# Kernel optimization log

Hardware: AMD Instinct MI355X
Metric: run time of the kernel (lower is better)

Reference implementation:

```python
import jax, jax.numpy as jnp
import numpy as np


def setup_inputs() -> dict:
    key = jax.random.key(0)
    k1, k2, k3 = jax.random.split(key, 3)
    B, C, H, W = 4, 3, 1024, 1920
    im0 = jax.random.normal(k1, (B, C, H, W), dtype=jnp.float32)
    # realistic optical-flow displacements of a few pixels
    flow = jax.random.normal(k2, (B, H, W, 2), dtype=jnp.float32) * 5.0
    flowback = jax.random.normal(k3, (B, H, W, 2), dtype=jnp.float32) * 5.0
    return {"im0": im0, "flow": flow, "flowback": flowback, "interpolation_mode": 0}


def _splat(im0, flow, interpolation_mode):
    # im0: [B,C,H,W], flow: [B,H,W,2] (dx, dy)
    B, C, H, W = im0.shape
    src = jnp.transpose(im0, (0, 2, 3, 1)).reshape(B * H * W, C)  # [BHW, C]
    gy, gx = jnp.meshgrid(jnp.arange(H, dtype=jnp.float32),
                          jnp.arange(W, dtype=jnp.float32), indexing="ij")
    x = gx[None] + flow[..., 0]  # [B,H,W] target x coord
    y = gy[None] + flow[..., 1]  # [B,H,W] target y coord
    b_idx = jnp.arange(B, dtype=jnp.int32)[:, None, None] * (H * W)  # batch offset

    out_flat = jnp.zeros((B * H * W, C), dtype=im0.dtype)

    if interpolation_mode == 1:  # Nearest
        xi = jnp.round(x).astype(jnp.int32)
        yi = jnp.round(y).astype(jnp.int32)
        corners = [(xi, yi, jnp.ones_like(x))]
    else:  # Bilinear: scatter-add to 4 neighbors
        x0 = jnp.floor(x).astype(jnp.int32)
        y0 = jnp.floor(y).astype(jnp.int32)
        x1, y1 = x0 + 1, y0 + 1
        x0f, y0f = x0.astype(x.dtype), y0.astype(y.dtype)
        wx1, wy1 = x - x0f, y - y0f
        wx0, wy0 = 1.0 - wx1, 1.0 - wy1
        corners = [(x0, y0, wx0 * wy0), (x1, y0, wx1 * wy0),
                   (x0, y1, wx0 * wy1), (x1, y1, wx1 * wy1)]

    for xi, yi, wgt in corners:
        valid = (xi >= 0) & (xi < W) & (yi >= 0) & (yi < H)
        w = wgt * valid.astype(im0.dtype)
        xc = jnp.clip(xi, 0, W - 1)
        yc = jnp.clip(yi, 0, H - 1)
        idx = (b_idx + yc * W + xc).reshape(-1)  # [BHW]
        out_flat = out_flat.at[idx].add(src * w.reshape(-1, 1))

    return jnp.transpose(out_flat.reshape(B, H, W, C), (0, 3, 1, 2))


def reference(im0, flow, flowback, interpolation_mode):
    # flowback is accepted (as in the CUDA extension signature) but the
    # forward splat itself only consumes im0 and the forward flow.
    return _splat(im0, flow, interpolation_mode)
```

## Files before the change

### kernel.cpp

```cpp
#include <hip/hip_runtime.h>

constexpr int B_ = 4;
constexpr int C_ = 3;
constexpr int H_ = 1024;
constexpr int W_ = 1920;
constexpr int HW_ = H_ * W_;

constexpr int TW = 128;
constexpr int TH = 64;
constexpr int R  = 16;
constexpr int EW = TW + 2 * R;
constexpr int EH = TH + 2 * R;
constexpr int ECELLS = EW * EH;

static_assert(W_ % TW == 0 && H_ % TH == 0, "exact tiling assumed");

__global__ __launch_bounds__(256) void forward_warp_tiled(
    const float* __restrict__ im0,
    const float2* __restrict__ flow,
    const int* __restrict__ mode_p,
    float* __restrict__ out) {
    __shared__ float tile[ECELLS];

    const int tx0 = blockIdx.x * TW;
    const int ty0 = blockIdx.y * TH;
    const int b   = blockIdx.z;
    const int mode = *mode_p;
    const int ex0 = tx0 - R;
    const int ey0 = ty0 - R;

    for (int c = 0; c < C_; ++c) {
        for (int i = threadIdx.x; i < ECELLS; i += 256) tile[i] = 0.0f;
        __syncthreads();

        const float* im0c = im0 + ((size_t)(b * C_ + c)) * HW_;
        float* outc = out + ((size_t)(b * C_ + c)) * HW_;

        for (int p = threadIdx.x; p < TW * TH; p += 256) {
            const int lx = p & (TW - 1);
            const int ly = p >> 7;
            const int x = tx0 + lx;
            const int y = ty0 + ly;
            const float2 f = flow[(size_t)(b * H_ + y) * W_ + x];
            const float s = im0c[y * W_ + x];
            const float px = (float)x + f.x;
            const float py = (float)y + f.y;

            int   cx[4], cy[4];
            float cw[4];
            int ncorn;
            if (mode == 1) {
                cx[0] = (int)rintf(px);
                cy[0] = (int)rintf(py);
                cw[0] = 1.0f;
                ncorn = 1;
            } else {
                const float xf = floorf(px), yf = floorf(py);
                const int x0 = (int)xf, y0i = (int)yf;
                const float wx1 = px - xf, wy1 = py - yf;
                const float wx0 = 1.0f - wx1, wy0 = 1.0f - wy1;
                cx[0] = x0;     cy[0] = y0i;     cw[0] = wx0 * wy0;
                cx[1] = x0 + 1; cy[1] = y0i;     cw[1] = wx1 * wy0;
                cx[2] = x0;     cy[2] = y0i + 1; cw[2] = wx0 * wy1;
                cx[3] = x0 + 1; cy[3] = y0i + 1; cw[3] = wx1 * wy1;
                ncorn = 4;
            }
            for (int k = 0; k < ncorn; ++k) {
                const int exi = cx[k] - ex0;
                const int eyi = cy[k] - ey0;
                const float v = s * cw[k];
                if ((unsigned)exi < (unsigned)EW && (unsigned)eyi < (unsigned)EH) {
                    atomicAdd(&tile[eyi * EW + exi], v);
                } else if ((unsigned)cx[k] < (unsigned)W_ &&
                           (unsigned)cy[k] < (unsigned)H_) {
                    unsafeAtomicAdd(outc + cy[k] * W_ + cx[k], v);
                }
            }
        }
        __syncthreads();

        for (int i = threadIdx.x; i < ECELLS; i += 256) {
            const float v = tile[i];
            if (v != 0.0f) {
                const int exi = i % EW;
                const int eyi = i / EW;
                const int gx = ex0 + exi;
                const int gy = ey0 + eyi;
                if ((unsigned)gx < (unsigned)W_ && (unsigned)gy < (unsigned)H_)
                    unsafeAtomicAdd(outc + gy * W_ + gx, v);
            }
        }
        __syncthreads();
    }
}

extern "C" void kernel_launch(void* const* d_in, const int* in_sizes, int n_in,
                              void* d_out, int out_size, void* d_ws, size_t ws_size,
                              hipStream_t stream) {
    const float*  im0  = (const float*)d_in[0];
    const float2* flow = (const float2*)d_in[1];
    const int*    mode = (const int*)d_in[3];
    float* out = (float*)d_out;

    (void)hipMemsetAsync(d_out, 0, (size_t)out_size * sizeof(float), stream);

    dim3 grid(W_ / TW, H_ / TH, B_);
    forward_warp_tiled<<<grid, dim3(256), 0, stream>>>(im0, flow, mode, out);
}
```

Baseline: 731.6 us.

## Template splat on mode, process two pixels per thread, shrink tile height

Specializes the kernel on interpolation mode via templates so the corner loop is fully unrolled, and has each thread load a float4 of flow and a float2 of image for two adjacent pixels. Tile clear and flush use float4 shared-memory accesses, skipping all-zero quads. Tile height is halved and launch bounds request 4 blocks per CU, aiming for more blocks and better latency hiding. In exchange the halo becomes a larger fraction of each tile, which adds global atomic flush traffic per pixel.

```diff
diff --git a/kernel.cpp b/kernel.cpp
--- a/kernel.cpp
+++ b/kernel.cpp
@@ -7,7 +7,7 @@
 constexpr int HW_ = H_ * W_;
 
 constexpr int TW = 128;
-constexpr int TH = 64;
+constexpr int TH = 32;
 constexpr int R  = 16;
 constexpr int EW = TW + 2 * R;
 constexpr int EH = TH + 2 * R;
@@ -15,95 +15,125 @@
 
 static_assert(W_ % TW == 0 && H_ % TH == 0, "exact tiling assumed");
 
-__global__ __launch_bounds__(256) void forward_warp_tiled(
-    const float* __restrict__ im0,
-    const float2* __restrict__ flow,
-    const int* __restrict__ mode_p,
-    float* __restrict__ out) {
-    __shared__ float tile[ECELLS];
+template <int MODE>
+__device__ __forceinline__ void splat_one(float* __restrict__ tile,
+                                          float* __restrict__ outc,
+                                          int ex0, int ey0,
+                                          int x, int y, float fx, float fy,
+                                          float s) {
+    const float px = (float)x + fx;
+    const float py = (float)y + fy;
+    if (MODE == 1) {
+        const int xi = (int)rintf(px);
+        const int yi = (int)rintf(py);
+        const int exi = xi - ex0, eyi = yi - ey0;
+        if ((unsigned)exi < (unsigned)EW && (unsigned)eyi < (unsigned)EH) {
+            atomicAdd(&tile[eyi * EW + exi], s);
+        } else if ((unsigned)xi < (unsigned)W_ && (unsigned)yi < (unsigned)H_) {
+            unsafeAtomicAdd(outc + yi * W_ + xi, s);
+        }
+    } else {
+        const float xf = floorf(px), yf = floorf(py);
+        const int x0 = (int)xf, y0 = (int)yf;
+        const float wx1 = px - xf, wy1 = py - yf;
+        const float wx0 = 1.0f - wx1, wy0 = 1.0f - wy1;
+        const int cx[4] = {x0, x0 + 1, x0, x0 + 1};
+        const int cy[4] = {y0, y0, y0 + 1, y0 + 1};
+        const float cw[4] = {wx0 * wy0, wx1 * wy0, wx0 * wy1, wx1 * wy1};
+#pragma unroll
+        for (int k = 0; k < 4; ++k) {
+            const int exi = cx[k] - ex0;
+            const int eyi = cy[k] - ey0;
+            const float v = s * cw[k];
+            if ((unsigned)exi < (unsigned)EW && (unsigned)eyi < (unsigned)EH) {
+                atomicAdd(&tile[eyi * EW + exi], v);
+            } else if ((unsigned)cx[k] < (unsigned)W_ &&
+                       (unsigned)cy[k] < (unsigned)H_) {
+                unsafeAtomicAdd(outc + cy[k] * W_ + cx[k], v);
+            }
+        }
+    }
+}
 
+template <int MODE>
+__device__ __forceinline__ void warp_body(const float* __restrict__ im0,
+                                          const float* __restrict__ flowf,
+                                          float* __restrict__ out,
+                                          float* __restrict__ tile) {
     const int tx0 = blockIdx.x * TW;
     const int ty0 = blockIdx.y * TH;
     const int b   = blockIdx.z;
-    const int mode = *mode_p;
     const int ex0 = tx0 - R;
     const int ey0 = ty0 - R;
 
+    float4* const tile4 = (float4*)tile;
+
     for (int c = 0; c < C_; ++c) {
-        for (int i = threadIdx.x; i < ECELLS; i += 256) tile[i] = 0.0f;
+        for (int v = threadIdx.x; v < ECELLS / 4; v += 256)
+            tile4[v] = make_float4(0.f, 0.f, 0.f, 0.f);
         __syncthreads();
 
         const float* im0c = im0 + ((size_t)(b * C_ + c)) * HW_;
         float* outc = out + ((size_t)(b * C_ + c)) * HW_;
 
-        for (int p = threadIdx.x; p < TW * TH; p += 256) {
-            const int lx = p & (TW - 1);
-            const int ly = p >> 7;
-            const int x = tx0 + lx;
+        for (int q = threadIdx.x; q < (TW * TH) / 2; q += 256) {
+            const int lp = q & 63;
+            const int ly = q >> 6;
+            const int x = tx0 + lp * 2;
             const int y = ty0 + ly;
-            const float2 f = flow[(size_t)(b * H_ + y) * W_ + x];
-            const float s = im0c[y * W_ + x];
-            const float px = (float)x + f.x;
-            const float py = (float)y + f.y;
-
-            int   cx[4], cy[4];
-            float cw[4];
-            int ncorn;
-            if (mode == 1) {
-                cx[0] = (int)rintf(px);
-                cy[0] = (int)rintf(py);
-                cw[0] = 1.0f;
-                ncorn = 1;
-            } else {
-                const float xf = floorf(px), yf = floorf(py);
-                const int x0 = (int)xf, y0i = (int)yf;
-                const float wx1 = px - xf, wy1 = py - yf;
-                const float wx0 = 1.0f - wx1, wy0 = 1.0f - wy1;
-                cx[0] = x0;     cy[0] = y0i;     cw[0] = wx0 * wy0;
-                cx[1] = x0 + 1; cy[1] = y0i;     cw[1] = wx1 * wy0;
-                cx[2] = x0;     cy[2] = y0i + 1; cw[2] = wx0 * wy1;
-                cx[3] = x0 + 1; cy[3] = y0i + 1; cw[3] = wx1 * wy1;
-                ncorn = 4;
-            }
-            for (int k = 0; k < ncorn; ++k) {
-                const int exi = cx[k] - ex0;
-                const int eyi = cy[k] - ey0;
-                const float v = s * cw[k];
-                if ((unsigned)exi < (unsigned)EW && (unsigned)eyi < (unsigned)EH) {
-                    atomicAdd(&tile[eyi * EW + exi], v);
-                } else if ((unsigned)cx[k] < (unsigned)W_ &&
-                           (unsigned)cy[k] < (unsigned)H_) {
-                    unsafeAtomicAdd(outc + cy[k] * W_ + cx[k], v);
-                }
-            }
+            const float4 f = *(const float4*)&flowf[((size_t)(b * H_ + y) * W_ + x) * 2];
+            const float2 s = *(const float2*)&im0c[y * W_ + x];
+            splat_one<MODE>(tile, outc, ex0, ey0, x,     y, f.x, f.y, s.x);
+            splat_one<MODE>(tile, outc, ex0, ey0, x + 1, y, f.z, f.w, s.y);
         }
         __syncthreads();
 
-        for (int i = threadIdx.x; i < ECELLS; i += 256) {
-            const float v = tile[i];
-            if (v != 0.0f) {
-                const int exi = i % EW;
-                const int eyi = i / EW;
-                const int gx = ex0 + exi;
-                const int gy = ey0 + eyi;
-                if ((unsigned)gx < (unsigned)W_ && (unsigned)gy < (unsigned)H_)
-                    unsafeAtomicAdd(outc + gy * W_ + gx, v);
+        for (int v = threadIdx.x; v < ECELLS / 4; v += 256) {
+            const float4 val = tile4[v];
+            if (val.x == 0.f && val.y == 0.f && val.z == 0.f && val.w == 0.f)
+                continue;
+            const int eyi = v / (EW / 4);
+            const int exi = (v - eyi * (EW / 4)) * 4;
+            const int gy = ey0 + eyi;
+            const int gx = ex0 + exi;
+            if ((unsigned)gy < (unsigned)H_) {
+                float* row = outc + gy * W_;
+                if (val.x != 0.f && (unsigned)(gx + 0) < (unsigned)W_)
+                    unsafeAtomicAdd(row + gx + 0, val.x);
+                if (val.y != 0.f && (unsigned)(gx + 1) < (unsigned)W_)
+                    unsafeAtomicAdd(row + gx + 1, val.y);
+                if (val.z != 0.f && (unsigned)(gx + 2) < (unsigned)W_)
+                    unsafeAtomicAdd(row + gx + 2, val.z);
+                if (val.w != 0.f && (unsigned)(gx + 3) < (unsigned)W_)
+                    unsafeAtomicAdd(row + gx + 3, val.w);
             }
         }
         __syncthreads();
     }
 }
 
+__global__ __launch_bounds__(256, 4) void forward_warp_tiled(
+    const float* __restrict__ im0,
+    const float* __restrict__ flowf,
+    const int* __restrict__ mode_p,
+    float* __restrict__ out) {
+    __shared__ float tile[ECELLS];
+    if (*mode_p == 1)
+        warp_body<1>(im0, flowf, out, tile);
+    else
+        warp_body<0>(im0, flowf, out, tile);
+}
+
 extern "C" void kernel_launch(void* const* d_in, const int* in_sizes, int n_in,
                               void* d_out, int out_size, void* d_ws, size_t ws_size,
                               hipStream_t stream) {
-    const float*  im0  = (const float*)d_in[0];
-    const float2* flow = (const float2*)d_in[1];
-    const int*    mode = (const int*)d_in[3];
+    const float* im0   = (const float*)d_in[0];
+    const float* flowf = (const float*)d_in[1];
+    const int*   mode  = (const int*)d_in[3];
     float* out = (float*)d_out;
 
     (void)hipMemsetAsync(d_out, 0, (size_t)out_size * sizeof(float), stream);
 
     dim3 grid(W_ / TW, H_ / TH, B_);
-    forward_warp_tiled<<<grid, dim3(256), 0, stream>>>(im0, flow, mode, out);
+    forward_warp_tiled<<<grid, dim3(256), 0, stream>>>(im0, flowf, mode, out);
 }
```

New measurement: 819.9 us. 1.12x slower.
